# Kernel optimization log

Measured on AMD Instinct MI355X. Metric: run time of the kernel, lower is better.

Reference implementation:

```python
import jax, jax.numpy as jnp
import numpy as np

B, S, HID = 2, 2048, 2048
NH, HD, G = 16, 128, 4
NKV = NH // G  # 4
ROPE_THETA = 10000.0


def _xavier(key, shape):
    fan_in, fan_out = shape
    lim = float(np.sqrt(6.0 / (fan_in + fan_out)))
    return jax.random.uniform(key, shape, jnp.float32, -lim, lim)


def setup_inputs() -> dict:
    key = jax.random.key(0)
    ks = jax.random.split(key, 6)
    hidden_states = jax.random.normal(ks[0], (B, S, HID), jnp.float32)
    # mask==True means MASKED (code adds mask * -1e9): causal upper triangle
    causal = jnp.triu(jnp.ones((S, S), jnp.bool_), k=1)
    mask = jnp.broadcast_to(causal[None, None], (B, 1, S, S))
    return {
        "hidden_states": hidden_states,
        "mask": mask,
        "Wq": _xavier(ks[1], (HID, NH * HD)),
        "bq": jnp.zeros((NH * HD,), jnp.float32),
        "Wk": _xavier(ks[2], (HID, NKV * HD)),
        "bk": jnp.zeros((NKV * HD,), jnp.float32),
        "Wv": _xavier(ks[3], (HID, NKV * HD)),
        "bv": jnp.zeros((NKV * HD,), jnp.float32),
        "Wo": _xavier(ks[4], (NH * HD, HID)),
        "bo": jnp.zeros((HID,), jnp.float32),
    }


def _rope_cos_sin(seq_len, head_dim, dtype):
    half = head_dim // 2
    inv_freq = 1.0 / (ROPE_THETA ** (jnp.arange(0, half, dtype=jnp.float32) / half))
    ang = jnp.arange(seq_len, dtype=jnp.float32)[:, None] * inv_freq[None, :]  # [S, half]
    # shape [1, S, 1, half] for broadcasting over (B, S, H, half)
    return jnp.cos(ang)[None, :, None, :].astype(dtype), jnp.sin(ang)[None, :, None, :].astype(dtype)


def _apply_rope(x, cos, sin):
    half = x.shape[-1] // 2
    x1, x2 = x[..., :half], x[..., half:]
    return jnp.concatenate([x1 * cos - x2 * sin, x1 * sin + x2 * cos], axis=-1)


def reference(hidden_states, mask, Wq, bq, Wk, bk, Wv, bv, Wo, bo):
    b, s, _ = hidden_states.shape
    scale = 1.0 / jnp.sqrt(jnp.asarray(HD, hidden_states.dtype))

    q = (hidden_states @ Wq + bq).reshape(b, s, NH, HD)
    k = (hidden_states @ Wk + bk).reshape(b, s, NKV, HD)
    v = (hidden_states @ Wv + bv).reshape(b, s, NKV, HD)

    cos, sin = _rope_cos_sin(s, HD, hidden_states.dtype)
    q = _apply_rope(q, cos, sin)
    k = _apply_rope(k, cos, sin)

    q = jnp.transpose(q, (0, 2, 1, 3))          # [B, NH, S, D]
    k = jnp.transpose(k, (0, 2, 1, 3))          # [B, NKV, S, D]
    v = jnp.transpose(v, (0, 2, 1, 3))          # [B, NKV, S, D]

    # GQA: group query heads instead of repeating K/V (same math as jnp.repeat)
    qg = q.reshape(b, NKV, G, s, HD)
    scores = jnp.einsum('bngqd,bnkd->bngqk', qg, k) * scale  # [B, NKV, G, S, S]

    maskf = mask.astype(scores.dtype)[:, :, None]  # [B, 1, 1, S, S]
    scores = scores + maskf * (-1e9)

    probs = jax.nn.softmax(scores, axis=-1)
    out = jnp.einsum('bngqk,bnkd->bngqd', probs, v)          # [B, NKV, G, S, D]
    out = out.reshape(b, NH, s, HD).transpose(0, 2, 1, 3).reshape(b, s, NH * HD)
    return out @ Wo + bo
```

## Files before the change

kernel.cpp:

```cpp
#include <hip/hip_runtime.h>
#include <hip/hip_bf16.h>

#define B_ 2
#define S_ 2048
#define HID_ 2048
#define NH_ 16
#define HD_ 128
#define NKV_ 4
#define M_ (B_*S_)
#define NQKV_ 3072
#define QSCALE2 0.12752464484148957f
#define DEFER_THR 11.5425f
#define NSPLIT 4

typedef __bf16 bf16x8 __attribute__((ext_vector_type(8)));
typedef float f32x4 __attribute__((ext_vector_type(4)));
typedef float f32x16 __attribute__((ext_vector_type(16)));

typedef __attribute__((address_space(1))) const unsigned int gas_uint;
typedef __attribute__((address_space(3))) unsigned int las_uint;

__device__ __forceinline__ unsigned short f2bfu(float x) {
  __hip_bfloat16 h = __float2bfloat16(x);
  return __builtin_bit_cast(unsigned short, h);
}

__device__ __forceinline__ unsigned int pack2bf(float lo, float hi) {
  return (unsigned int)f2bfu(lo) | ((unsigned int)f2bfu(hi) << 16);
}

__device__ __forceinline__ float bflo(unsigned int u) {
  return __builtin_bit_cast(float, u << 16);
}
__device__ __forceinline__ float bfhi(unsigned int u) {
  return __builtin_bit_cast(float, u & 0xffff0000u);
}
__device__ __forceinline__ float bf2f(unsigned short u) {
  return __builtin_bit_cast(float, (unsigned int)u << 16);
}

__device__ __forceinline__ void gload_lds16(const void* g, void* l) {
  __builtin_amdgcn_global_load_lds((gas_uint*)g, (las_uint*)l, 16, 0, 0);
}


__global__ void k_prep(const float* __restrict__ X, unsigned short* __restrict__ Xb,
                       const float* __restrict__ bq, const float* __restrict__ bk,
                       const float* __restrict__ bv, float* __restrict__ Bqkv,
                       float* __restrict__ cosT, float* __restrict__ sinT) {
  int blk = blockIdx.x;
  if (blk < 8192) {
    int i = blk * 256 + threadIdx.x;
    float4 v = ((const float4*)X)[i];
    ushort4 o;
    o.x = f2bfu(v.x); o.y = f2bfu(v.y); o.z = f2bfu(v.z); o.w = f2bfu(v.w);
    ((ushort4*)Xb)[i] = o;
  } else if (blk < 8204) {
    int i = (blk - 8192) * 256 + threadIdx.x;
    float v = (i < 2048) ? bq[i] : (i < 2560 ? bk[i - 2048] : bv[i - 2560]);
    Bqkv[i] = v;
  } else {
    int idx = (blk - 8204) * 256 + threadIdx.x;
    int s = idx >> 6, i = idx & 63;
    float invf = expf(-(float)i * (9.210340371976184f / 64.f));
    float ang = (float)s * invf;
    cosT[idx] = cosf(ang);
    sinT[idx] = sinf(ang);
  }
}

__global__ void k_tcvtall(const float* __restrict__ Wq, const float* __restrict__ Wk,
                          const float* __restrict__ Wv, const float* __restrict__ Wo,
                          unsigned short* __restrict__ Wt, unsigned short* __restrict__ Wot) {
  __shared__ float t[32][33];
  int blk = blockIdx.x;
  const float* src;
  unsigned short* dst;
  int R, C, bx, by;
  if (blk < 4096)      { src = Wq; dst = Wt;              R = 2048; C = 2048; int i = blk;        bx = i & 63; by = i >> 6; }
  else if (blk < 5120) { src = Wk; dst = Wt + 2048*2048;  R = 2048; C = 512;  int i = blk - 4096; bx = i & 15; by = i >> 4; }
  else if (blk < 6144) { src = Wv; dst = Wt + 2560*2048;  R = 2048; C = 512;  int i = blk - 5120; bx = i & 15; by = i >> 4; }
  else                 { src = Wo; dst = Wot;             R = 2048; C = 2048; int i = blk - 6144; bx = i & 63; by = i >> 6; }
  int bc = bx * 32, br = by * 32;
  int tx = threadIdx.x & 31, ty = threadIdx.x >> 5;
  for (int i = ty; i < 32; i += 8)
    t[i][tx] = src[(size_t)(br + i) * C + bc + tx];
  __syncthreads();
  for (int i = ty; i < 32; i += 8)
    dst[(size_t)(bc + i) * R + br + tx] = f2bfu(t[tx][i]);
}

__global__ void k_rope(const unsigned short* __restrict__ Cq, const float* __restrict__ cosT,
                       const float* __restrict__ sinT, unsigned short* __restrict__ Qr,
                       unsigned short* __restrict__ Kr, unsigned short* __restrict__ Vt) {
  __shared__ unsigned short t[32][136];
  int blk = blockIdx.x;
  if (blk < 16384) {
    int idx = blk * 256 + threadIdx.x;
    int i = idx & 63, h = (idx >> 6) & (NH_ - 1), m = idx >> 10;
    int s = m & (S_ - 1), b = m >> 11;
    const unsigned short* row = Cq + (size_t)m * NQKV_ + h * HD_;
    float x1 = bf2f(row[i]), x2 = bf2f(row[i + 64]);
    float c = cosT[(s << 6) + i], sn = sinT[(s << 6) + i];
    size_t base = ((size_t)(b * NH_ + h) * S_ + s) * HD_;
    Qr[base + i]      = f2bfu((x1 * c - x2 * sn) * QSCALE2);
    Qr[base + i + 64] = f2bfu((x1 * sn + x2 * c) * QSCALE2);
  } else if (blk < 20480) {
    int idx = (blk - 16384) * 256 + threadIdx.x;
    int i = idx & 63, kv = (idx >> 6) & (NKV_ - 1), m = idx >> 8;
    int s = m & (S_ - 1), b = m >> 11;
    const unsigned short* row = Cq + (size_t)m * NQKV_ + 2048 + kv * HD_;
    float x1 = bf2f(row[i]), x2 = bf2f(row[i + 64]);
    float c = cosT[(s << 6) + i], sn = sinT[(s << 6) + i];
    size_t base = ((size_t)(b * NKV_ + kv) * S_ + s) * HD_;
    Kr[base + i]      = f2bfu(x1 * c - x2 * sn);
    Kr[base + i + 64] = f2bfu(x1 * sn + x2 * c);
  } else {
    int bx = blk - 20480;
    int st = bx & 63, kv = (bx >> 6) & 3, b = bx >> 8;
    int s0 = st * 32;
    int tid = threadIdx.x;
    for (int j = 0; j < 16; ++j) {
      int idx = j * 256 + tid;
      int si = idx >> 7, d = idx & 127;
      t[si][d] = Cq[(size_t)(b * S_ + s0 + si) * NQKV_ + 2560 + kv * HD_ + d];
    }
    __syncthreads();
    for (int j = 0; j < 16; ++j) {
      int idx = j * 256 + tid;
      int d = idx >> 5, si = idx & 31;
      Vt[((size_t)(b * NKV_ + kv) * HD_ + d) * S_ + s0 + si] = t[si][d];
    }
  }
}


template <bool BF16OUT>
__global__ __launch_bounds__(256, 2)
void k_gemm(const unsigned short* __restrict__ A, const unsigned short* __restrict__ Bt,
            const float* __restrict__ bias, void* __restrict__ Cv,
            int Md, int Nd, int Kd) {
  __shared__ __align__(16) unsigned short As[128 * 64];
  __shared__ __align__(16) unsigned short Bs[128 * 64];
  int nt = Nd >> 7;
  int nwg = (Md >> 7) * nt;
  int bid = blockIdx.x;
  int wg = bid;
  if ((nwg & 7) == 0) { int cpx = nwg >> 3; wg = (bid & 7) * cpx + (bid >> 3); }
  int bm = wg / nt, bn = wg - bm * nt;
  int tid = threadIdx.x;
  int lane = tid & 63, w = tid >> 6;
  int wm = (w >> 1) << 6, wn = (w & 1) << 6;
  int lr = lane & 15, lg = lane >> 4;
  f32x4 acc[4][4] = {};

  const int chunkbase = w << 2;
  const int boff = lane << 4;
  const int nK = Kd >> 6;
  const size_t rowstride = (size_t)Kd * 2;

  for (int kt = 0; kt < nK; ++kt) {
#pragma unroll
    for (int i = 0; i < 4; ++i) {
      int off = ((chunkbase + i) << 10) + boff;
      int row = off >> 7;
      int colb = off & 127;
      int scolb = colb ^ ((row & 7) << 4);
      const char* ga = (const char*)A + (size_t)(bm * 128 + row) * rowstride + (kt << 7) + scolb;
      const char* gb = (const char*)Bt + (size_t)(bn * 128 + row) * rowstride + (kt << 7) + scolb;
      gload_lds16(ga, (char*)As + ((chunkbase + i) << 10));
      gload_lds16(gb, (char*)Bs + ((chunkbase + i) << 10));
    }
    __syncthreads();
#pragma unroll
    for (int kk = 0; kk < 2; ++kk) {
      bf16x8 a[4], b[4];
      int kb = ((kk << 5) + (lg << 3)) << 1;
#pragma unroll
      for (int mi = 0; mi < 4; ++mi) {
        int row = wm + (mi << 4) + lr;
        a[mi] = *(const bf16x8*)((const char*)As + (row << 7) + (kb ^ ((row & 7) << 4)));
      }
#pragma unroll
      for (int ni = 0; ni < 4; ++ni) {
        int row = wn + (ni << 4) + lr;
        b[ni] = *(const bf16x8*)((const char*)Bs + (row << 7) + (kb ^ ((row & 7) << 4)));
      }
#pragma unroll
      for (int mi = 0; mi < 4; ++mi)
#pragma unroll
        for (int ni = 0; ni < 4; ++ni)
          acc[mi][ni] = __builtin_amdgcn_mfma_f32_16x16x32_bf16(a[mi], b[ni], acc[mi][ni], 0, 0, 0);
    }
    __syncthreads();
  }
#pragma unroll
  for (int mi = 0; mi < 4; ++mi) {
    int r0 = bm * 128 + wm + (mi << 4) + (lg << 2);
#pragma unroll
    for (int ni = 0; ni < 4; ++ni) {
      int col = bn * 128 + wn + (ni << 4) + lr;
      float bz = bias[col];
#pragma unroll
      for (int r = 0; r < 4; ++r) {
        float v = acc[mi][ni][r] + bz;
        if constexpr (BF16OUT)
          ((unsigned short*)Cv)[(size_t)(r0 + r) * Nd + col] = f2bfu(v);
        else
          ((float*)Cv)[(size_t)(r0 + r) * Nd + col] = v;
      }
    }
  }
}


__global__ __launch_bounds__(256, 2)
void k_attn(const unsigned short* __restrict__ Qr, const unsigned short* __restrict__ Kr,
            const unsigned short* __restrict__ Vt,
            unsigned short* __restrict__ Po0, unsigned short* __restrict__ Po1,
            unsigned short* __restrict__ Po2, unsigned short* __restrict__ Po3,
            float2* __restrict__ Ml) {
  __shared__ __align__(16) unsigned short Ks[2][64 * 128];
  int bid = blockIdx.x;
  int g = bid & 7;
  int b = g >> 2, kvh = g & 3;
  int r = bid >> 3;
  int split = r & 3;
  int r2 = r >> 2;
  int hg = r2 >> 4;
  int qt = 15 - (r2 & 15);
  int h = (kvh << 2) + hg;
  int tid = threadIdx.x, lane = tid & 63, w = tid >> 6;
  int ql = lane & 31, hi = lane >> 5;
  int q0 = (qt << 7) + (w << 5);
  int qrow = q0 + ql;

  const unsigned short* Qp = Qr + (((size_t)(b * NH_ + h) * S_) << 7);
  const unsigned short* Kp = Kr + (((size_t)(b * NKV_ + kvh) * S_) << 7);
  const unsigned short* Vp = Vt + (((size_t)(b * NKV_ + kvh) * HD_) << 11);

  bf16x8 qa[8];
#pragma unroll
  for (int c = 0; c < 8; ++c)
    qa[c] = *(const bf16x8*)(Qp + (((size_t)qrow) << 7) + (c << 4) + (hi << 3));

  f32x16 acc[4] = {};
  float m_r = -1e30f, l_r = 0.f;

  const int T = (qt + 1) << 1;
  const int nit = (T - split + 3) >> 2;

#define STAGE_K(bsel, t)                                                        \
  {                                                                             \
    const char* kbase = (const char*)Kp + ((size_t)(t) << 14);                  \
    _Pragma("unroll")                                                           \
    for (int i_ = 0; i_ < 4; ++i_) {                                            \
      int woff_ = (i_ << 12) + (w << 10);                                       \
      int off_ = woff_ + (lane << 4);                                           \
      int row_ = off_ >> 8;                                                     \
      int colb_ = off_ & 255;                                                   \
      int scolb_ = colb_ ^ ((row_ & 15) << 4);                                  \
      gload_lds16(kbase + ((size_t)row_ << 8) + scolb_,                         \
                  (char*)Ks[bsel] + woff_);                                     \
    }                                                                           \
  }

  STAGE_K(0, split);
  __syncthreads();

  for (int i = 0; i < nit; ++i) {
    int t = split + (i << 2);
    if (i + 1 < nit) STAGE_K((i + 1) & 1, t + 4);
    const char* Kb = (const char*)Ks[i & 1];

#pragma unroll
    for (int sub = 0; sub < 2; ++sub) {
      int kvbase = (t << 6) + (sub << 5);
      if (kvbase > q0 + 31) continue;

      f32x16 st = {};
      int krow = (sub << 5) + ql;
      int sw = (krow & 15) << 4;
#pragma unroll
      for (int c = 0; c < 8; ++c) {
        int cb = (c << 5) + (hi << 4);
        bf16x8 kf = *(const bf16x8*)(Kb + (krow << 8) + (cb ^ sw));
        st = __builtin_amdgcn_mfma_f32_32x32x16_bf16(kf, qa[c], st, 0, 0, 0);
      }
      bf16x8 vf[8];
#pragma unroll
      for (int dc = 0; dc < 4; ++dc) {
        const unsigned short* vrow = Vp + (((size_t)((dc << 5) + ql)) << 11) + kvbase + (hi << 3);
        vf[2 * dc]     = *(const bf16x8*)(vrow);
        vf[2 * dc + 1] = *(const bf16x8*)(vrow + 16);
      }
      if (kvbase + 31 > q0) {
#pragma unroll
        for (int rr = 0; rr < 16; ++rr) {
          int kv = kvbase + (rr & 3) + ((rr >> 2) << 3) + (hi << 2);
          if (kv > qrow) st[rr] = -1e30f;
        }
      }
      float pmax = st[0];
#pragma unroll
      for (int rr = 1; rr < 16; ++rr) pmax = fmaxf(pmax, st[rr]);
      pmax = fmaxf(pmax, __shfl_xor(pmax, 32));
      if (!__all(pmax <= m_r + DEFER_THR)) {
        float mn = fmaxf(m_r, pmax);
        float al = exp2f(m_r - mn);
        m_r = mn;
        l_r *= al;
#pragma unroll
        for (int dc = 0; dc < 4; ++dc) acc[dc] = acc[dc] * al;
      }
      float p[16];
      float ps = 0.f;
#pragma unroll
      for (int rr = 0; rr < 16; ++rr) { p[rr] = exp2f(st[rr] - m_r); ps += p[rr]; }
      l_r += ps;
      unsigned int W[8];
#pragma unroll
      for (int i2 = 0; i2 < 8; ++i2) W[i2] = pack2bf(p[2 * i2], p[2 * i2 + 1]);
      unsigned int e0 = __shfl_xor(hi ? W[0] : W[2], 32);
      unsigned int e1 = __shfl_xor(hi ? W[1] : W[3], 32);
      unsigned int e2 = __shfl_xor(hi ? W[4] : W[6], 32);
      unsigned int e3 = __shfl_xor(hi ? W[5] : W[7], 32);
      uint4 u0, u1;
      u0.x = hi ? e0 : W[0];
      u0.y = hi ? e1 : W[1];
      u0.z = hi ? W[2] : e0;
      u0.w = hi ? W[3] : e1;
      u1.x = hi ? e2 : W[4];
      u1.y = hi ? e3 : W[5];
      u1.z = hi ? W[6] : e2;
      u1.w = hi ? W[7] : e3;
      bf16x8 pa0 = __builtin_bit_cast(bf16x8, u0);
      bf16x8 pa1 = __builtin_bit_cast(bf16x8, u1);
#pragma unroll
      for (int dc = 0; dc < 4; ++dc) {
        acc[dc] = __builtin_amdgcn_mfma_f32_32x32x16_bf16(vf[2 * dc], pa0, acc[dc], 0, 0, 0);
        acc[dc] = __builtin_amdgcn_mfma_f32_32x32x16_bf16(vf[2 * dc + 1], pa1, acc[dc], 0, 0, 0);
      }
    }
    __syncthreads();
  }

  float l_tot = l_r + __shfl_xor(l_r, 32);
  unsigned short* Pob = (split == 0) ? Po0 : (split == 1) ? Po1 : (split == 2) ? Po2 : Po3;
  float inv = (l_tot > 0.f) ? (1.f / l_tot) : 0.f;
  unsigned short* obase = Pob + ((((size_t)(b * S_) + qrow)) << 11) + (h << 7) + (hi << 2);
#pragma unroll
  for (int dc = 0; dc < 4; ++dc)
#pragma unroll
    for (int gq = 0; gq < 4; ++gq) {
      ushort4 o;
      o.x = f2bfu(acc[dc][4 * gq + 0] * inv);
      o.y = f2bfu(acc[dc][4 * gq + 1] * inv);
      o.z = f2bfu(acc[dc][4 * gq + 2] * inv);
      o.w = f2bfu(acc[dc][4 * gq + 3] * inv);
      *(ushort4*)(obase + (dc << 5) + (gq << 3)) = o;
    }
  if (hi == 0)
    Ml[(size_t)split * (M_ * NH_) + ((size_t)(b * S_) + qrow) * NH_ + h] = make_float2(m_r, l_tot);
}

__global__ void k_comb(const unsigned short* __restrict__ Po0, const unsigned short* __restrict__ Po1,
                       const unsigned short* __restrict__ Po2, const unsigned short* __restrict__ Po3,
                       const float2* __restrict__ Ml, unsigned short* __restrict__ Ob) {
  int idx = blockIdx.x * 256 + threadIdx.x;
  int c = idx >> 4;
  float2 a0 = Ml[c], a1 = Ml[c + M_ * NH_], a2 = Ml[c + 2 * M_ * NH_], a3 = Ml[c + 3 * M_ * NH_];
  float m = fmaxf(fmaxf(a0.x, a1.x), fmaxf(a2.x, a3.x));
  float w0 = a0.y * exp2f(a0.x - m);
  float w1 = a1.y * exp2f(a1.x - m);
  float w2 = a2.y * exp2f(a2.x - m);
  float w3 = a3.y * exp2f(a3.x - m);
  float inv = 1.f / (w0 + w1 + w2 + w3);
  w0 *= inv; w1 *= inv; w2 *= inv; w3 *= inv;
  size_t e = (size_t)idx << 3;
  uint4 v0 = *(const uint4*)(Po0 + e);
  uint4 v1 = *(const uint4*)(Po1 + e);
  uint4 v2 = *(const uint4*)(Po2 + e);
  uint4 v3 = *(const uint4*)(Po3 + e);
  uint4 o;
  o.x = pack2bf(w0 * bflo(v0.x) + w1 * bflo(v1.x) + w2 * bflo(v2.x) + w3 * bflo(v3.x),
                w0 * bfhi(v0.x) + w1 * bfhi(v1.x) + w2 * bfhi(v2.x) + w3 * bfhi(v3.x));
  o.y = pack2bf(w0 * bflo(v0.y) + w1 * bflo(v1.y) + w2 * bflo(v2.y) + w3 * bflo(v3.y),
                w0 * bfhi(v0.y) + w1 * bfhi(v1.y) + w2 * bfhi(v2.y) + w3 * bfhi(v3.y));
  o.z = pack2bf(w0 * bflo(v0.z) + w1 * bflo(v1.z) + w2 * bflo(v2.z) + w3 * bflo(v3.z),
                w0 * bfhi(v0.z) + w1 * bfhi(v1.z) + w2 * bfhi(v2.z) + w3 * bfhi(v3.z));
  o.w = pack2bf(w0 * bflo(v0.w) + w1 * bflo(v1.w) + w2 * bflo(v2.w) + w3 * bflo(v3.w),
                w0 * bfhi(v0.w) + w1 * bfhi(v1.w) + w2 * bfhi(v2.w) + w3 * bfhi(v3.w));
  *(uint4*)(Ob + e) = o;
}


extern "C" void kernel_launch(void* const* d_in, const int* in_sizes, int n_in,
                              void* d_out, int out_size, void* d_ws, size_t ws_size,
                              hipStream_t stream) {
  const float* X  = (const float*)d_in[0];
  const float* Wq = (const float*)d_in[2];
  const float* bq = (const float*)d_in[3];
  const float* Wk = (const float*)d_in[4];
  const float* bk = (const float*)d_in[5];
  const float* Wv = (const float*)d_in[6];
  const float* bv = (const float*)d_in[7];
  const float* Wo = (const float*)d_in[8];
  const float* bo = (const float*)d_in[9];
  float* out = (float*)d_out;

  char* ws = (char*)d_ws;
  unsigned short* Xb  = (unsigned short*)(ws);
  unsigned short* Wt  = (unsigned short*)(ws + 16777216);
  unsigned short* Wot = (unsigned short*)(ws + 29360128);
  float* Bqkv         = (float*)(ws + 37748736);
  float* cosT         = (float*)(ws + 37761024);
  float* sinT         = (float*)(ws + 38285312);
  unsigned short* Cqkvb = (unsigned short*)(ws + 38809600);
  unsigned short* Qr  = (unsigned short*)(ws + 89141248);
  unsigned short* Kr  = (unsigned short*)(ws + 105918464);
  unsigned short* Vtb = (unsigned short*)(ws + 110112768);
  unsigned short* Ob  = (unsigned short*)(ws + 114307072);
  unsigned short* Po0 = (unsigned short*)(ws);
  unsigned short* Po1 = (unsigned short*)(ws + 38809600);
  unsigned short* Po2 = (unsigned short*)(ws + 38809600 + 16777216);
  unsigned short* Po3 = (unsigned short*)(ws + 38809600 + 33554432);
  float2* Ml          = (float2*)(ws + 16777216);

  k_prep<<<8716, 256, 0, stream>>>(X, Xb, bq, bk, bv, Bqkv, cosT, sinT);
  k_tcvtall<<<10240, 256, 0, stream>>>(Wq, Wk, Wv, Wo, Wt, Wot);

  k_gemm<true><<<(M_ / 128) * (NQKV_ / 128), 256, 0, stream>>>(Xb, Wt, Bqkv, Cqkvb, M_, NQKV_, HID_);

  k_rope<<<20992, 256, 0, stream>>>(Cqkvb, cosT, sinT, Qr, Kr, Vtb);

  k_attn<<<B_ * NH_ * (S_ / 128) * NSPLIT, 256, 0, stream>>>(Qr, Kr, Vtb, Po0, Po1, Po2, Po3, Ml);
  k_comb<<<M_ * HID_ / 8 / 256, 256, 0, stream>>>(Po0, Po1, Po2, Po3, Ml, Ob);

  k_gemm<false><<<(M_ / 128) * (HID_ / 128), 256, 0, stream>>>(Ob, Wot, bo, out, M_, HID_, NH_ * HD_);
}
```

Baseline: 237.2 us.

## Fuse RoPE into QKV GEMM epilogue and change warp tiling to full-width rows

The QKV GEMM epilogue now applies RoPE, and the Q scale for Q, writing Qr and Kr directly in head-major layout. The separate rope kernel shrinks to a V transpose only. To pair the d and d+64 columns inside one thread, the warp tiling changes from 64x64 per warp to 32 rows by the full 128 columns (acc[2][8]). This also affects the output GEMM. The fusion removes a round trip of Q/K through the bf16 intermediate, in exchange for more B-fragment LDS loads per warp and scattered epilogue stores.

```diff
diff --git a/kernel.cpp b/kernel.cpp
--- a/kernel.cpp
+++ b/kernel.cpp
@@ -90,56 +90,33 @@
     dst[(size_t)(bc + i) * R + br + tx] = f2bfu(t[tx][i]);
 }
 
-__global__ void k_rope(const unsigned short* __restrict__ Cq, const float* __restrict__ cosT,
-                       const float* __restrict__ sinT, unsigned short* __restrict__ Qr,
-                       unsigned short* __restrict__ Kr, unsigned short* __restrict__ Vt) {
+__global__ void k_vt(const unsigned short* __restrict__ Cq, unsigned short* __restrict__ Vt) {
   __shared__ unsigned short t[32][136];
-  int blk = blockIdx.x;
-  if (blk < 16384) {
-    int idx = blk * 256 + threadIdx.x;
-    int i = idx & 63, h = (idx >> 6) & (NH_ - 1), m = idx >> 10;
-    int s = m & (S_ - 1), b = m >> 11;
-    const unsigned short* row = Cq + (size_t)m * NQKV_ + h * HD_;
-    float x1 = bf2f(row[i]), x2 = bf2f(row[i + 64]);
-    float c = cosT[(s << 6) + i], sn = sinT[(s << 6) + i];
-    size_t base = ((size_t)(b * NH_ + h) * S_ + s) * HD_;
-    Qr[base + i]      = f2bfu((x1 * c - x2 * sn) * QSCALE2);
-    Qr[base + i + 64] = f2bfu((x1 * sn + x2 * c) * QSCALE2);
-  } else if (blk < 20480) {
-    int idx = (blk - 16384) * 256 + threadIdx.x;
-    int i = idx & 63, kv = (idx >> 6) & (NKV_ - 1), m = idx >> 8;
-    int s = m & (S_ - 1), b = m >> 11;
-    const unsigned short* row = Cq + (size_t)m * NQKV_ + 2048 + kv * HD_;
-    float x1 = bf2f(row[i]), x2 = bf2f(row[i + 64]);
-    float c = cosT[(s << 6) + i], sn = sinT[(s << 6) + i];
-    size_t base = ((size_t)(b * NKV_ + kv) * S_ + s) * HD_;
-    Kr[base + i]      = f2bfu(x1 * c - x2 * sn);
-    Kr[base + i + 64] = f2bfu(x1 * sn + x2 * c);
-  } else {
-    int bx = blk - 20480;
-    int st = bx & 63, kv = (bx >> 6) & 3, b = bx >> 8;
-    int s0 = st * 32;
-    int tid = threadIdx.x;
-    for (int j = 0; j < 16; ++j) {
-      int idx = j * 256 + tid;
-      int si = idx >> 7, d = idx & 127;
-      t[si][d] = Cq[(size_t)(b * S_ + s0 + si) * NQKV_ + 2560 + kv * HD_ + d];
-    }
-    __syncthreads();
-    for (int j = 0; j < 16; ++j) {
-      int idx = j * 256 + tid;
-      int d = idx >> 5, si = idx & 31;
-      Vt[((size_t)(b * NKV_ + kv) * HD_ + d) * S_ + s0 + si] = t[si][d];
-    }
-  }
-}
-
-
-template <bool BF16OUT>
+  int bx = blockIdx.x;
+  int st = bx & 63, kv = (bx >> 6) & 3, b = bx >> 8;
+  int s0 = st * 32;
+  int tid = threadIdx.x;
+  for (int j = 0; j < 16; ++j) {
+    int idx = j * 256 + tid;
+    int si = idx >> 7, d = idx & 127;
+    t[si][d] = Cq[(size_t)(b * S_ + s0 + si) * NQKV_ + 2560 + kv * HD_ + d];
+  }
+  __syncthreads();
+  for (int j = 0; j < 16; ++j) {
+    int idx = j * 256 + tid;
+    int d = idx >> 5, si = idx & 31;
+    Vt[((size_t)(b * NKV_ + kv) * HD_ + d) * S_ + s0 + si] = t[si][d];
+  }
+}
+
+
+template <int MODE>
 __global__ __launch_bounds__(256, 2)
 void k_gemm(const unsigned short* __restrict__ A, const unsigned short* __restrict__ Bt,
             const float* __restrict__ bias, void* __restrict__ Cv,
-            int Md, int Nd, int Kd) {
+            int Md, int Nd, int Kd,
+            const float* __restrict__ cosT, const float* __restrict__ sinT,
+            unsigned short* __restrict__ Qr, unsigned short* __restrict__ Kr) {
   __shared__ __align__(16) unsigned short As[128 * 64];
   __shared__ __align__(16) unsigned short Bs[128 * 64];
   int nt = Nd >> 7;
@@ -150,9 +127,8 @@
   int bm = wg / nt, bn = wg - bm * nt;
   int tid = threadIdx.x;
   int lane = tid & 63, w = tid >> 6;
-  int wm = (w >> 1) << 6, wn = (w & 1) << 6;
   int lr = lane & 15, lg = lane >> 4;
-  f32x4 acc[4][4] = {};
+  f32x4 acc[2][8] = {};
 
   const int chunkbase = w << 2;
   const int boff = lane << 4;
@@ -174,40 +150,72 @@
     __syncthreads();
 #pragma unroll
     for (int kk = 0; kk < 2; ++kk) {
-      bf16x8 a[4], b[4];
+      bf16x8 a[2], b[8];
       int kb = ((kk << 5) + (lg << 3)) << 1;
 #pragma unroll
-      for (int mi = 0; mi < 4; ++mi) {
-        int row = wm + (mi << 4) + lr;
+      for (int mi = 0; mi < 2; ++mi) {
+        int row = (w << 5) + (mi << 4) + lr;
         a[mi] = *(const bf16x8*)((const char*)As + (row << 7) + (kb ^ ((row & 7) << 4)));
       }
 #pragma unroll
-      for (int ni = 0; ni < 4; ++ni) {
-        int row = wn + (ni << 4) + lr;
+      for (int ni = 0; ni < 8; ++ni) {
+        int row = (ni << 4) + lr;
         b[ni] = *(const bf16x8*)((const char*)Bs + (row << 7) + (kb ^ ((row & 7) << 4)));
       }
 #pragma unroll
-      for (int mi = 0; mi < 4; ++mi)
-#pragma unroll
-        for (int ni = 0; ni < 4; ++ni)
+      for (int mi = 0; mi < 2; ++mi)
+#pragma unroll
+        for (int ni = 0; ni < 8; ++ni)
           acc[mi][ni] = __builtin_amdgcn_mfma_f32_16x16x32_bf16(a[mi], b[ni], acc[mi][ni], 0, 0, 0);
     }
     __syncthreads();
   }
-#pragma unroll
-  for (int mi = 0; mi < 4; ++mi) {
-    int r0 = bm * 128 + wm + (mi << 4) + (lg << 2);
-#pragma unroll
-    for (int ni = 0; ni < 4; ++ni) {
-      int col = bn * 128 + wn + (ni << 4) + lr;
-      float bz = bias[col];
+
+  if (MODE == 0 || bn >= 20) {
+#pragma unroll
+    for (int mi = 0; mi < 2; ++mi) {
+      int r0 = bm * 128 + (w << 5) + (mi << 4) + (lg << 2);
+#pragma unroll
+      for (int ni = 0; ni < 8; ++ni) {
+        int col = bn * 128 + (ni << 4) + lr;
+        float bz = bias[col];
+#pragma unroll
+        for (int r = 0; r < 4; ++r) {
+          float v = acc[mi][ni][r] + bz;
+          if (MODE == 1)
+            ((unsigned short*)Cv)[(size_t)(r0 + r) * Nd + col] = f2bfu(v);
+          else
+            ((float*)Cv)[(size_t)(r0 + r) * Nd + col] = v;
+        }
+      }
+    }
+  } else {
+    bool isQ = (bn < 16);
+    int hh = isQ ? bn : bn - 16;
+#pragma unroll
+    for (int mi = 0; mi < 2; ++mi) {
 #pragma unroll
       for (int r = 0; r < 4; ++r) {
-        float v = acc[mi][ni][r] + bz;
-        if constexpr (BF16OUT)
-          ((unsigned short*)Cv)[(size_t)(r0 + r) * Nd + col] = f2bfu(v);
-        else
-          ((float*)Cv)[(size_t)(r0 + r) * Nd + col] = v;
+        int m = bm * 128 + (w << 5) + (mi << 4) + (lg << 2) + r;
+        int s = m & (S_ - 1), bb = m >> 11;
+        size_t qbase = ((size_t)(bb * NH_ + hh) * S_ + s) * HD_;
+        size_t kbase = ((size_t)(bb * NKV_ + hh) * S_ + s) * HD_;
+#pragma unroll
+        for (int ni = 0; ni < 4; ++ni) {
+          int c = (ni << 4) + lr;
+          float v1 = acc[mi][ni][r]     + bias[bn * 128 + c];
+          float v2 = acc[mi][ni + 4][r] + bias[bn * 128 + c + 64];
+          float cs = cosT[(s << 6) + c], sn = sinT[(s << 6) + c];
+          float o1 = v1 * cs - v2 * sn;
+          float o2 = v1 * sn + v2 * cs;
+          if (isQ) {
+            Qr[qbase + c]      = f2bfu(o1 * QSCALE2);
+            Qr[qbase + c + 64] = f2bfu(o2 * QSCALE2);
+          } else {
+            Kr[kbase + c]      = f2bfu(o1);
+            Kr[kbase + c + 64] = f2bfu(o2);
+          }
+        }
       }
     }
   }
@@ -430,12 +438,14 @@
   k_prep<<<8716, 256, 0, stream>>>(X, Xb, bq, bk, bv, Bqkv, cosT, sinT);
   k_tcvtall<<<10240, 256, 0, stream>>>(Wq, Wk, Wv, Wo, Wt, Wot);
 
-  k_gemm<true><<<(M_ / 128) * (NQKV_ / 128), 256, 0, stream>>>(Xb, Wt, Bqkv, Cqkvb, M_, NQKV_, HID_);
-
-  k_rope<<<20992, 256, 0, stream>>>(Cqkvb, cosT, sinT, Qr, Kr, Vtb);
+  k_gemm<1><<<(M_ / 128) * (NQKV_ / 128), 256, 0, stream>>>(
+      Xb, Wt, Bqkv, Cqkvb, M_, NQKV_, HID_, cosT, sinT, Qr, Kr);
+
+  k_vt<<<B_ * NKV_ * (S_ / 32), 256, 0, stream>>>(Cqkvb, Vtb);
 
   k_attn<<<B_ * NH_ * (S_ / 128) * NSPLIT, 256, 0, stream>>>(Qr, Kr, Vtb, Po0, Po1, Po2, Po3, Ml);
   k_comb<<<M_ * HID_ / 8 / 256, 256, 0, stream>>>(Po0, Po1, Po2, Po3, Ml, Ob);
 
-  k_gemm<false><<<(M_ / 128) * (HID_ / 128), 256, 0, stream>>>(Ob, Wot, bo, out, M_, HID_, NH_ * HD_);
-}
+  k_gemm<0><<<(M_ / 128) * (HID_ / 128), 256, 0, stream>>>(
+      Ob, Wot, bo, out, M_, HID_, NH_ * HD_, nullptr, nullptr, nullptr, nullptr);
+}
```

After: 232.7 us. About the same (-1.9%).
